# Kernel optimization log

Hardware: AMD Instinct MI355X
Metric: run time of the kernel (lower is better)

Reference implementation:

```python
import jax, jax.numpy as jnp
import numpy as np

# Static config (matches init_kwargs)
B = 1
D = 1024          # model_dim
H = 16            # num_heads
HD = 64           # head_dim
TPF = 256         # tokens_per_frame = latent_height*latent_width
LH, LW = 16, 16
FRAMES = 13
PREFIX = 1
ATTN = 3
CHUNKS = 4
TXT = 226                 # text_length per chunk
SEQ_TXT = CHUNKS * TXT    # 904
VID_LEN = FRAMES * TPF    # 3328
CHUNK_VID = (PREFIX + ATTN) * TPF  # 1024 video tokens per attention chunk
THETA = 10000.0
EPS = 1e-6
SCALE = 1.0 / np.sqrt(HD)
DT, DHE, DW = 16, 24, 24  # 3D rope split of head_dim


def setup_inputs() -> dict:
    key = jax.random.key(0)
    ks = jax.random.split(key, 16)
    def w(k, shape, s=0.02):
        return (jax.random.normal(k, shape) * s).astype(jnp.float32)
    return dict(
        vid_emb=jax.random.normal(ks[0], (B, VID_LEN, D), jnp.float32),
        text_emb=jax.random.normal(ks[1], (B, SEQ_TXT, D), jnp.float32),
        Wq=w(ks[2], (D, D)), bq=jnp.zeros((D,), jnp.float32),
        Wk=w(ks[3], (D, D)), bk=jnp.zeros((D,), jnp.float32),
        Wv=w(ks[4], (D, D)), bv=jnp.zeros((D,), jnp.float32),
        Wo=w(ks[5], (D, D)), bo=jnp.zeros((D,), jnp.float32),
        qn_w=jnp.ones((HD,), jnp.float32), qn_b=jnp.zeros((HD,), jnp.float32),
        kn_w=jnp.ones((HD,), jnp.float32), kn_b=jnp.zeros((HD,), jnp.float32),
        ssm_Win=w(ks[6], (D, D)), ssm_Wout=w(ks[7], (D, D)),
        ssm_gate=jnp.zeros((D,), jnp.float32),
        fg_t=jnp.full((D,), 0.1, jnp.float32), fg_v=jnp.full((D,), 0.1, jnp.float32),
        bg_t=jnp.full((D,), 0.1, jnp.float32), bg_v=jnp.full((D,), 0.1, jnp.float32),
    )


def _layernorm(x, w, b):
    mu = jnp.mean(x, axis=-1, keepdims=True)
    var = jnp.mean((x - mu) ** 2, axis=-1, keepdims=True)
    return (x - mu) * jax.lax.rsqrt(var + EPS) * w + b


def _rope_angles():
    # per-video-token 3D positions within a chunk
    tok = jnp.arange(CHUNK_VID)
    f = (tok // TPF).astype(jnp.float32)
    rem = tok % TPF
    hp = (rem // LW).astype(jnp.float32)
    wp = (rem % LW).astype(jnp.float32)
    def inv(d):
        return THETA ** (-jnp.arange(0, d, 2, dtype=jnp.float32) / d)
    return f[:, None] * inv(DT), hp[:, None] * inv(DHE), wp[:, None] * inv(DW)


def _rot(x, ang):
    half = x.shape[-1] // 2
    c, s = jnp.cos(ang), jnp.sin(ang)
    x1, x2 = x[..., :half], x[..., half:]
    return jnp.concatenate([x1 * c - x2 * s, x1 * s + x2 * c], axis=-1)


def _apply_rope3d(x, angs):
    at, ah, aw = angs
    return jnp.concatenate([
        _rot(x[..., :DT], at),
        _rot(x[..., DT:DT + DHE], ah),
        _rot(x[..., DT + DHE:], aw),
    ], axis=-1)


def _attn_forward(vid_emb, text_emb, Wq, bq, Wk, bk, Wv, bv, Wo, bo, qn_w, qn_b, kn_w, kn_b):
    b = vid_emb.shape[0]
    starts = np.arange(CHUNKS) * ATTN * TPF
    idx = jnp.asarray(starts)[:, None] + jnp.arange(CHUNK_VID)[None, :]  # [C, CHUNK_VID]
    txt_chunks = text_emb.reshape(b, CHUNKS, TXT, D)
    vid_chunks = vid_emb[:, idx]                                          # [b, C, CHUNK_VID, D]
    cur = jnp.concatenate([txt_chunks, vid_chunks], axis=2)               # [b, C, T, D]
    T = TXT + CHUNK_VID
    cur = cur.reshape(b * CHUNKS, T, D)

    def heads(x):
        return x.reshape(b * CHUNKS, T, H, HD).transpose(0, 2, 1, 3)      # [bc, h, t, d]

    q = _layernorm(heads(cur @ Wq + bq), qn_w, qn_b)
    k = _layernorm(heads(cur @ Wk + bk), kn_w, kn_b)
    v = heads(cur @ Wv + bv)

    angs = _rope_angles()
    q = jnp.concatenate([q[:, :, :TXT], _apply_rope3d(q[:, :, TXT:], angs)], axis=2)
    k = jnp.concatenate([k[:, :, :TXT], _apply_rope3d(k[:, :, TXT:], angs)], axis=2)

    scores = jnp.einsum('bhqd,bhkd->bhqk', q, k) * SCALE
    attn = jax.nn.softmax(scores, axis=-1)
    out = jnp.einsum('bhqk,bhkd->bhqd', attn, v)
    out = out.transpose(0, 2, 1, 3).reshape(b * CHUNKS, T, D) @ Wo + bo
    out = out.reshape(b, CHUNKS, T, D)

    text_out = out[:, :, :TXT].reshape(b, SEQ_TXT, D)
    vid_part = out[:, :, TXT:]                                            # [b, C, CHUNK_VID, D]
    vid_acc = jnp.zeros((b, VID_LEN, D), vid_emb.dtype).at[:, idx].add(vid_part)
    cnt = jnp.zeros((b, VID_LEN, 1), vid_emb.dtype).at[:, idx].add(jnp.ones((b, CHUNKS, CHUNK_VID, 1), vid_emb.dtype))
    vid_out = vid_acc / cnt
    return jnp.concatenate([text_out, vid_out], axis=1)


def _ssm(x, Win, Wout, gate_logit):
    # simplified TTT stand-in: gated linear recurrence h_t = g*h_{t-1} + u_t (causal scan)
    g = jax.nn.sigmoid(gate_logit)
    u = x @ Win
    a = jnp.broadcast_to(g, u.shape)
    def comb(c1, c2):
        a1, b1 = c1
        a2, b2 = c2
        return a1 * a2, a2 * b1 + b2
    _, h = jax.lax.associative_scan(comb, (a, u), axis=1)
    return h @ Wout


def _rev_text_chunks(t):
    b = t.shape[0]
    return jnp.flip(t.reshape(b, CHUNKS, TXT, D), axis=1).reshape(b, SEQ_TXT, D)


def _ssm_forward(emb, ssm_Win, ssm_Wout, ssm_gate, fg_t, fg_v, bg_t, bg_v):
    Ttxt = SEQ_TXT
    res = emb
    y = _ssm(emb, ssm_Win, ssm_Wout, ssm_gate)
    emb = res + jnp.concatenate([jnp.tanh(fg_t) * y[:, :Ttxt], jnp.tanh(fg_v) * y[:, Ttxt:]], axis=1)
    res2 = emb
    # multiscene reverse: flip text chunk order and video token order
    rev = jnp.concatenate([_rev_text_chunks(emb[:, :Ttxt]), jnp.flip(emb[:, Ttxt:], axis=1)], axis=1)
    y2 = _ssm(rev, ssm_Win, ssm_Wout, ssm_gate)
    y2 = jnp.concatenate([_rev_text_chunks(y2[:, :Ttxt]), jnp.flip(y2[:, Ttxt:], axis=1)], axis=1)
    return res2 + jnp.concatenate([jnp.tanh(bg_t) * y2[:, :Ttxt], jnp.tanh(bg_v) * y2[:, Ttxt:]], axis=1)


def reference(vid_emb, text_emb, Wq, bq, Wk, bk, Wv, bv, Wo, bo, qn_w, qn_b, kn_w, kn_b,
              ssm_Win, ssm_Wout, ssm_gate, fg_t, fg_v, bg_t, bg_v):
    emb = _attn_forward(vid_emb, text_emb, Wq, bq, Wk, bk, Wv, bv, Wo, bo, qn_w, qn_b, kn_w, kn_b)
    out = _ssm_forward(emb, ssm_Win, ssm_Wout, ssm_gate, fg_t, fg_v, bg_t, bg_v)
    return out[:, SEQ_TXT:], out[:, :SEQ_TXT]
```

## Files before the change

### kernel.cpp

```cpp
#include <hip/hip_runtime.h>
#include <cstdint>

constexpr int Dm       = 1024;
constexpr int Hh       = 16;
constexpr int HD       = 64;
constexpr int CHUNKS   = 4;
constexpr int TXT      = 226;
constexpr int SEQ_TXT  = 904;
constexpr int VID_LEN  = 3328;
constexpr int CHUNK_VID= 1024;
constexpr int Tt       = 1250;
constexpr int Tp       = 1280;
constexpr int M_QKV    = 5000;
constexpr int SEQm     = 4232;
constexpr int STRIDE_V = 768;
constexpr float EPSc   = 1e-6f;
constexpr float SCALEc = 0.125f;
constexpr float OFFS   = 8.0f;
constexpr float C16    = 1.6609640474f;
constexpr float C24    = 1.1073093649f;

constexpr int SEGL2 = 64;
constexpr int HALO  = 64;
constexpr int NSEG2 = (SEQm + SEGL2 - 1) / SEGL2;

typedef __attribute__((ext_vector_type(8))) short bf16x8;
typedef __attribute__((ext_vector_type(4))) float f32x4;

__device__ __forceinline__ ushort f2bf(float x) {
    uint32_t u = __float_as_uint(x);
    u += 0x7FFFu + ((u >> 16) & 1u);
    return (ushort)(u >> 16);
}
__device__ __forceinline__ float bf2f(ushort b) {
    return __uint_as_float(((uint32_t)b) << 16);
}

__device__ __forceinline__ void gload_lds16(const ushort* g, ushort* l) {
    __builtin_amdgcn_global_load_lds(
        (const __attribute__((address_space(1))) unsigned int*)g,
        (__attribute__((address_space(3))) unsigned int*)l, 16, 0, 0);
}

__device__ __forceinline__ int rev_map(int i) {
    if (i < SEQ_TXT) {
        int c = i / TXT, o = i - c * TXT;
        return (CHUNKS - 1 - c) * TXT + o;
    }
    int j = i - SEQ_TXT;
    return SEQ_TXT + (VID_LEN - 1 - j);
}

__global__ __launch_bounds__(256) void prep_all(
    const float* __restrict__ Wq, const float* __restrict__ Wk,
    const float* __restrict__ Wv, const float* __restrict__ Wo,
    const float* __restrict__ Win, const float* __restrict__ Wout,
    const float* __restrict__ vid, const float* __restrict__ txt,
    ushort* __restrict__ WqkvH, ushort* __restrict__ WqkvL,
    ushort* __restrict__ WoH, ushort* __restrict__ WoL,
    ushort* __restrict__ WinH, ushort* __restrict__ WinL,
    ushort* __restrict__ WoutH, ushort* __restrict__ WoutL,
    ushort* __restrict__ chi, ushort* __restrict__ clo) {
    __shared__ float tile[32][33];
    if (blockIdx.z == 6) {
        int base = (blockIdx.y * 32 + blockIdx.x) * 256 + threadIdx.x;
        for (int idx = base; idx < M_QKV * 256; idx += 32 * 32 * 256) {
            int row = idx >> 8, c4 = (idx & 255) * 4;
            int c = row / Tt, t = row - c * Tt;
            float4 x;
            if (t < TXT)
                x = *(const float4*)(txt + (size_t)(c * TXT + t) * Dm + c4);
            else
                x = *(const float4*)(vid + (size_t)(c * STRIDE_V + (t - TXT)) * Dm + c4);
            float v[4] = {x.x, x.y, x.z, x.w};
            ushort4 h, l;
            h.x = f2bf(v[0]); l.x = f2bf(v[0] - bf2f(h.x));
            h.y = f2bf(v[1]); l.y = f2bf(v[1] - bf2f(h.y));
            h.z = f2bf(v[2]); l.z = f2bf(v[2] - bf2f(h.z));
            h.w = f2bf(v[3]); l.w = f2bf(v[3] - bf2f(h.w));
            *(ushort4*)(chi + (size_t)row * Dm + c4) = h;
            *(ushort4*)(clo + (size_t)row * Dm + c4) = l;
        }
        return;
    }
    const float* W; ushort* Thi; ushort* Tlo;
    switch (blockIdx.z) {
        case 0: W = Wq;  Thi = WqkvH;               Tlo = WqkvL;               break;
        case 1: W = Wk;  Thi = WqkvH + 1024*1024;   Tlo = WqkvL + 1024*1024;   break;
        case 2: W = Wv;  Thi = WqkvH + 2*1024*1024; Tlo = WqkvL + 2*1024*1024; break;
        case 3: W = Wo;  Thi = WoH;   Tlo = WoL;   break;
        case 4: W = Win; Thi = WinH;  Tlo = WinL;  break;
        default:W = Wout;Thi = WoutH; Tlo = WoutL; break;
    }
    int k0 = blockIdx.y * 32, n0 = blockIdx.x * 32;
    int j = threadIdx.x & 31, i0 = threadIdx.x >> 5;
#pragma unroll
    for (int i = i0; i < 32; i += 8)
        tile[i][j] = W[(size_t)(k0 + i) * 1024 + n0 + j];
    __syncthreads();
#pragma unroll
    for (int i = i0; i < 32; i += 8) {
        float v = tile[j][i];
        ushort h = f2bf(v);
        size_t o = (size_t)(n0 + i) * 1024 + k0 + j;
        Thi[o] = h;
        Tlo[o] = f2bf(v - bf2f(h));
    }
}

template<int MODE>
__global__ __launch_bounds__(256) void gemm_sk(
    const ushort* __restrict__ Ahi, const ushort* __restrict__ Alo,
    const ushort* __restrict__ Bhi, const ushort* __restrict__ Blo,
    const float* __restrict__ f1, const float* __restrict__ f2,
    const float* __restrict__ f3,
    float* __restrict__ Cf, ushort* __restrict__ u1,
    int M, int N) {
    __shared__ ushort AHL[128 * 64];
    __shared__ ushort BHL[128 * 64];
    const int tid = threadIdx.x;
    const int w = tid >> 6, lane = tid & 63;
    const int lrow = lane & 15, quad = lane >> 4;
    const int mBase = blockIdx.y * 128, nBase = blockIdx.x * 128;

    const bool isB = (w >= 2);
    const int half = w & 1;
    const ushort* Phi = isB ? Bhi : Ahi;
    const ushort* Plo = isB ? Blo : Alo;
    ushort* lds = (isB ? BHL : AHL) + half * 4096;
    const int baseR = (isB ? nBase : mBase) + half * 64;
    const int maxr = (isB ? N : M) - 1;
    const int rl8 = lane >> 3;
    const int c = (lane & 7) ^ rl8;
    const ushort* Psel = (c < 4) ? Phi : Plo;
    const ushort* gb[8];
#pragma unroll
    for (int u = 0; u < 8; ++u) {
        int rg = min(baseR + u * 8 + rl8, maxr);
        gb[u] = Psel + (size_t)rg * 1024 + (c & 3) * 8;
    }

    const int mo = (w >> 1) * 64, no = (w & 1) * 64;
    const int p = quad ^ (lrow & 7);
    f32x4 acc[4][4];
#pragma unroll
    for (int i = 0; i < 4; ++i)
#pragma unroll
        for (int j = 0; j < 4; ++j) acc[i][j] = (f32x4){0.f, 0.f, 0.f, 0.f};

    const int kk0 = (MODE == 5) ? blockIdx.z * 512 : 0;
    const int kk1 = (MODE == 5) ? kk0 + 512 : 1024;
    for (int kk = kk0; kk < kk1; kk += 32) {
        __syncthreads();
#pragma unroll
        for (int u = 0; u < 8; ++u) gload_lds16(gb[u] + kk, lds + u * 512);
        __syncthreads();

        bf16x8 ah[4], al[4], bh[4], bl[4];
#pragma unroll
        for (int i = 0; i < 4; ++i) {
            int m = mo + i * 16 + lrow;
            ah[i] = *(const bf16x8*)&AHL[m * 64 + p * 8];
            al[i] = *(const bf16x8*)&AHL[m * 64 + (p ^ 4) * 8];
        }
#pragma unroll
        for (int j = 0; j < 4; ++j) {
            int n = no + j * 16 + lrow;
            bh[j] = *(const bf16x8*)&BHL[n * 64 + p * 8];
            bl[j] = *(const bf16x8*)&BHL[n * 64 + (p ^ 4) * 8];
        }
#pragma unroll
        for (int i = 0; i < 4; ++i)
#pragma unroll
            for (int j = 0; j < 4; ++j) {
                f32x4 a = acc[i][j];
                a = __builtin_amdgcn_mfma_f32_16x16x32_bf16(ah[i], bh[j], a, 0, 0, 0);
                a = __builtin_amdgcn_mfma_f32_16x16x32_bf16(al[i], bh[j], a, 0, 0, 0);
                a = __builtin_amdgcn_mfma_f32_16x16x32_bf16(ah[i], bl[j], a, 0, 0, 0);
                acc[i][j] = a;
            }
    }

    const size_t zoff = (MODE == 5) ? (size_t)blockIdx.z * M * N : 0;
#pragma unroll
    for (int i = 0; i < 4; ++i)
#pragma unroll
        for (int j = 0; j < 4; ++j) {
            const int col = nBase + no + j * 16 + lrow;
            float bv = 0.f;
            if constexpr (MODE == 1)
                bv = (col < 1024) ? f1[col]
                   : (col < 2048) ? f2[col - 1024] : f3[col - 2048];
#pragma unroll
            for (int r = 0; r < 4; ++r) {
                const int row = mBase + mo + i * 16 + quad * 4 + r;
                if (row >= M) continue;
                const size_t idx = (size_t)row * N + col;
                const float a = acc[i][j][r];
                if constexpr (MODE == 1) {
                    u1[idx] = f2bf(a + bv);
                } else {
                    Cf[zoff + idx] = a;
                }
            }
        }
}

__global__ __launch_bounds__(256) void lnrope(
    const ushort* __restrict__ qkvb,
    const float* __restrict__ qn_w, const float* __restrict__ qn_b,
    const float* __restrict__ kn_w, const float* __restrict__ kn_b,
    ushort* __restrict__ qP, ushort* __restrict__ kP, ushort* __restrict__ vT) {
    __shared__ ushort vtile[64][72];
    const int ch = blockIdx.y, c = ch >> 4, h = ch & 15;
    const int t0 = blockIdx.x * 64;
    const int tid = threadIdx.x, w = tid >> 6, lane = tid & 63;

    auto wsum = [](float x) {
#pragma unroll
        for (int o = 32; o; o >>= 1) x += __shfl_xor(x, o);
        return x;
    };

#pragma unroll 1
    for (int it = 0; it < 16; ++it) {
        const int tl = w * 16 + it;
        const int t = t0 + tl;
        ushort qb = 0, kb = 0, vb = 0;
        if (t < Tt) {
            size_t src = (size_t)(c * Tt + t) * 3072 + h * HD + lane;
            float qv = bf2f(qkvb[src]);
            float kv = bf2f(qkvb[src + 1024]);
            float vv = bf2f(qkvb[src + 2048]);

            float qmu = wsum(qv) * (1.f / 64.f);
            float qd  = qv - qmu;
            float qvar = wsum(qd * qd) * (1.f / 64.f);
            float qn = qd * rsqrtf(qvar + EPSc) * qn_w[lane] + qn_b[lane];

            float kmu = wsum(kv) * (1.f / 64.f);
            float kd  = kv - kmu;
            float kvar = wsum(kd * kd) * (1.f / 64.f);
            float kn = kd * rsqrtf(kvar + EPSc) * kn_w[lane] + kn_b[lane];

            if (t >= TXT) {
                int pos = t - TXT;
                int f = pos >> 8, rem2 = pos & 255, hp = rem2 >> 4, wp = rem2 & 15;
                int p, dl; float cc;
                if (lane < 16)      { cc = C16; p = f;  dl = lane; }
                else if (lane < 40) { cc = C24; p = hp; dl = lane - 16; }
                else                { cc = C24; p = wp; dl = lane - 40; }
                int halfd = (lane < 16) ? 8 : 12;
                int i = (dl < halfd) ? dl : dl - halfd;
                float ang = (float)p * exp2f(-(float)i * cc);
                float cs = cosf(ang), sn = sinf(ang);
                int partner = (dl < halfd) ? (lane + halfd) : (lane - halfd);
                float qo = __shfl(qn, partner);
                float ko = __shfl(kn, partner);
                qn = (dl < halfd) ? (qn * cs - qo * sn) : (qo * sn + qn * cs);
                kn = (dl < halfd) ? (kn * cs - ko * sn) : (ko * sn + kn * cs);
            }
            qb = f2bf(qn * SCALEc);
            kb = f2bf(kn);
            vb = f2bf(vv);
        }
        size_t dst = ((size_t)ch * Tp + t) * HD + lane;
        qP[dst] = qb;
        kP[dst] = kb;
        vtile[tl][lane] = vb;
    }
    __syncthreads();
    const int r = tid >> 2, ck = tid & 3;
    ushort* dst = vT + ((size_t)ch * HD + r) * Tp + t0;
    short o1[8], o2[8];
#pragma unroll
    for (int j = 0; j < 8; ++j) {
        o1[j] = (short)vtile[ck * 8 + j][r];
        o2[j] = (short)vtile[(ck + 4) * 8 + j][r];
    }
    *(bf16x8*)(dst + ck * 8)       = *(bf16x8*)o1;
    *(bf16x8*)(dst + (ck + 4) * 8) = *(bf16x8*)o2;
}

__global__ __launch_bounds__(256) void attn_mfma(
    const ushort* __restrict__ qP, const ushort* __restrict__ kP,
    const ushort* __restrict__ vT,
    ushort* __restrict__ ohi, ushort* __restrict__ olo) {
    const int ch = blockIdx.y;
    const int c = ch >> 4, h = ch & 15;
    const int qbase = blockIdx.x * 64;
    const int tid = threadIdx.x, w = tid >> 6, lane = tid & 63;
    const int lrow = lane & 15, quad = lane >> 4;

    __shared__ ushort KT[2][32 * 64];
    __shared__ ushort VTs[2][64 * 32];
    __shared__ ushort PB[4][16][40];

    const ushort* kg = kP + (size_t)ch * Tp * HD;
    const ushort* vg = vT + (size_t)ch * HD * Tp;

    const ushort* kgl = kg + (size_t)(w * 8 + (lane >> 3)) * HD
                           + ((lane & 7) ^ ((lane >> 3) & 7)) * 8;
    const ushort* vgl = vg + (size_t)(w * 16 + (lane >> 2)) * Tp + (lane & 3) * 8;

    const int qr = qbase + w * 16 + lrow;
    const ushort* qgp = qP + ((size_t)ch * Tp + qr) * HD + quad * 8;
    bf16x8 qf0 = *(const bf16x8*)qgp;
    bf16x8 qf1 = *(const bf16x8*)(qgp + 32);

    f32x4 accO[4];
#pragma unroll
    for (int dt = 0; dt < 4; ++dt) accO[dt] = (f32x4){0.f, 0.f, 0.f, 0.f};
    float lacc[4] = {0.f, 0.f, 0.f, 0.f};

    gload_lds16(kgl, &KT[0][w * 512]);
    gload_lds16(vgl, &VTs[0][w * 512]);

    const int NSTEP = Tp / 32;
    for (int s = 0; s < NSTEP; ++s) {
        const int b = s & 1;
        __syncthreads();
        if (s + 1 < NSTEP) {
            int kb = (s + 1) * 32;
            gload_lds16(kgl + (size_t)kb * HD, &KT[1 - b][w * 512]);
            gload_lds16(vgl + kb, &VTs[1 - b][w * 512]);
        }

        const int sw = lrow & 7;
        const ushort* r0 = &KT[b][lrow * 64];
        const ushort* r1 = &KT[b][(16 + lrow) * 64];
        bf16x8 k00 = *(const bf16x8*)(r0 + (quad ^ sw) * 8);
        bf16x8 k01 = *(const bf16x8*)(r0 + ((4 + quad) ^ sw) * 8);
        bf16x8 k10 = *(const bf16x8*)(r1 + (quad ^ sw) * 8);
        bf16x8 k11 = *(const bf16x8*)(r1 + ((4 + quad) ^ sw) * 8);
        f32x4 s0 = (f32x4){0.f, 0.f, 0.f, 0.f}, s1 = s0;
        s0 = __builtin_amdgcn_mfma_f32_16x16x32_bf16(qf0, k00, s0, 0, 0, 0);
        s0 = __builtin_amdgcn_mfma_f32_16x16x32_bf16(qf1, k01, s0, 0, 0, 0);
        s1 = __builtin_amdgcn_mfma_f32_16x16x32_bf16(qf0, k10, s1, 0, 0, 0);
        s1 = __builtin_amdgcn_mfma_f32_16x16x32_bf16(qf1, k11, s1, 0, 0, 0);

#pragma unroll
        for (int r = 0; r < 4; ++r) {
            float p0 = __expf(s0[r] - OFFS);
            float p1 = __expf(s1[r] - OFFS);
            lacc[r] += p0 + p1;
            int row = quad * 4 + r;
            PB[w][row][lrow]      = f2bf(p0);
            PB[w][row][16 + lrow] = f2bf(p1);
        }

        bf16x8 pf = *(const bf16x8*)&PB[w][lrow][quad * 8];
#pragma unroll
        for (int dt = 0; dt < 4; ++dt) {
            bf16x8 vf = *(const bf16x8*)&VTs[b][(dt * 16 + lrow) * 32 + quad * 8];
            accO[dt] = __builtin_amdgcn_mfma_f32_16x16x32_bf16(pf, vf, accO[dt], 0, 0, 0);
        }
    }

    float il[4];
#pragma unroll
    for (int r = 0; r < 4; ++r) {
        float l = lacc[r];
        l += __shfl_xor(l, 1);
        l += __shfl_xor(l, 2);
        l += __shfl_xor(l, 4);
        l += __shfl_xor(l, 8);
        l -= (float)(Tp - Tt) * __expf(-OFFS);
        il[r] = 1.f / l;
    }
#pragma unroll
    for (int dt = 0; dt < 4; ++dt)
#pragma unroll
        for (int r = 0; r < 4; ++r) {
            int qrow = qbase + w * 16 + quad * 4 + r;
            if (qrow < Tt) {
                float val = accO[dt][r] * il[r];
                size_t o = (size_t)(c * Tt + qrow) * Dm + h * HD + dt * 16 + lrow;
                ushort hv = f2bf(val);
                ohi[o] = hv;
                olo[o] = f2bf(val - bf2f(hv));
            }
        }
}

__global__ __launch_bounds__(256) void reduce_scatter(
    const float* __restrict__ P0, const float* __restrict__ bo,
    ushort* __restrict__ ehi, ushort* __restrict__ elo) {
    const float* P1 = P0 + (size_t)M_QKV * Dm;
    int idx = blockIdx.x * 256 + threadIdx.x;
    int row = idx >> 8, c4 = (idx & 255) * 4;
    float sx, sy, sz, sw;
    if (row < SEQ_TXT) {
        int c = row / TXT, t = row - c * TXT;
        size_t o = (size_t)(c * Tt + t) * Dm + c4;
        float4 a = *(const float4*)(P0 + o);
        float4 b = *(const float4*)(P1 + o);
        sx = a.x + b.x; sy = a.y + b.y; sz = a.z + b.z; sw = a.w + b.w;
    } else {
        int p = row - SEQ_TXT;
        sx = sy = sz = sw = 0.f; int cnt = 0;
#pragma unroll
        for (int c = 0; c < CHUNKS; ++c) {
            int off = p - c * STRIDE_V;
            if (off >= 0 && off < CHUNK_VID) {
                size_t o = (size_t)(c * Tt + TXT + off) * Dm + c4;
                float4 a = *(const float4*)(P0 + o);
                float4 b = *(const float4*)(P1 + o);
                sx += a.x + b.x; sy += a.y + b.y;
                sz += a.z + b.z; sw += a.w + b.w;
                ++cnt;
            }
        }
        float inv = 1.f / (float)cnt;
        sx *= inv; sy *= inv; sz *= inv; sw *= inv;
    }
    float4 b4 = *(const float4*)(bo + c4);
    float v[4] = {sx + b4.x, sy + b4.y, sz + b4.z, sw + b4.w};
    ushort4 h, l;
    h.x = f2bf(v[0]); l.x = f2bf(v[0] - bf2f(h.x));
    h.y = f2bf(v[1]); l.y = f2bf(v[1] - bf2f(h.y));
    h.z = f2bf(v[2]); l.z = f2bf(v[2] - bf2f(h.z));
    h.w = f2bf(v[3]); l.w = f2bf(v[3] - bf2f(h.w));
    *(ushort4*)(ehi + (size_t)row * Dm + c4) = h;
    *(ushort4*)(elo + (size_t)row * Dm + c4) = l;
}

__global__ __launch_bounds__(256) void scan_halo(
    const float* __restrict__ P0, const float* __restrict__ gate,
    ushort* __restrict__ hhi, ushort* __restrict__ hlo, int perm) {
    const float* P1 = P0 + (size_t)SEQm * Dm;
    int ch = blockIdx.x * 256 + threadIdx.x;
    int seg = blockIdx.y;
    float g = 1.f / (1.f + expf(-gate[ch]));
    int tw0 = seg * SEGL2;
    int tw1 = min(SEQm, tw0 + SEGL2);
    int t0 = max(0, tw0 - HALO);
    float hv = 0.f;
    for (int t = t0; t < tw0; ++t) {
        int rt = perm ? rev_map(t) : t;
        size_t o = (size_t)rt * Dm + ch;
        hv = fmaf(g, hv, P0[o] + P1[o]);
    }
    for (int t = tw0; t < tw1; ++t) {
        int rt = perm ? rev_map(t) : t;
        size_t o = (size_t)rt * Dm + ch;
        hv = fmaf(g, hv, P0[o] + P1[o]);
        ushort h = f2bf(hv);
        hhi[o] = h;
        hlo[o] = f2bf(hv - bf2f(h));
    }
}

__global__ __launch_bounds__(256) void reduce_c1(
    const float* __restrict__ P0,
    const ushort* __restrict__ ehi, const ushort* __restrict__ elo,
    const float* __restrict__ fg_t, const float* __restrict__ fg_v,
    float* __restrict__ emb2, ushort* __restrict__ e2hi, ushort* __restrict__ e2lo) {
    const float* P1 = P0 + (size_t)SEQm * Dm;
    int idx = blockIdx.x * 256 + threadIdx.x;
    int row = idx >> 8, c4 = (idx & 255) * 4;
    const float* fg = (row < SEQ_TXT) ? fg_t : fg_v;
    size_t o = (size_t)row * Dm + c4;
    float4 a = *(const float4*)(P0 + o);
    float4 b = *(const float4*)(P1 + o);
    ushort4 eh = *(const ushort4*)(ehi + o);
    ushort4 el = *(const ushort4*)(elo + o);
    float v[4];
    v[0] = (bf2f(eh.x) + bf2f(el.x)) + tanhf(fg[c4 + 0]) * (a.x + b.x);
    v[1] = (bf2f(eh.y) + bf2f(el.y)) + tanhf(fg[c4 + 1]) * (a.y + b.y);
    v[2] = (bf2f(eh.z) + bf2f(el.z)) + tanhf(fg[c4 + 2]) * (a.z + b.z);
    v[3] = (bf2f(eh.w) + bf2f(el.w)) + tanhf(fg[c4 + 3]) * (a.w + b.w);
    *(float4*)(emb2 + o) = make_float4(v[0], v[1], v[2], v[3]);
    ushort4 h, l;
    h.x = f2bf(v[0]); l.x = f2bf(v[0] - bf2f(h.x));
    h.y = f2bf(v[1]); l.y = f2bf(v[1] - bf2f(h.y));
    h.z = f2bf(v[2]); l.z = f2bf(v[2] - bf2f(h.z));
    h.w = f2bf(v[3]); l.w = f2bf(v[3] - bf2f(h.w));
    *(ushort4*)(e2hi + o) = h;
    *(ushort4*)(e2lo + o) = l;
}

__global__ __launch_bounds__(256) void reduce_fin(
    const float* __restrict__ P0, const float* __restrict__ emb2,
    const float* __restrict__ bg_t, const float* __restrict__ bg_v,
    float* __restrict__ outp) {
    const float* P1 = P0 + (size_t)SEQm * Dm;
    int idx = blockIdx.x * 256 + threadIdx.x;
    int row = idx >> 8, c4 = (idx & 255) * 4;
    const float* bg = (row < SEQ_TXT) ? bg_t : bg_v;
    int drow = (row >= SEQ_TXT) ? (row - SEQ_TXT) : (VID_LEN + row);
    size_t o = (size_t)row * Dm + c4;
    float4 a = *(const float4*)(P0 + o);
    float4 b = *(const float4*)(P1 + o);
    float4 e = *(const float4*)(emb2 + o);
    float4 r = make_float4(e.x + tanhf(bg[c4 + 0]) * (a.x + b.x),
                           e.y + tanhf(bg[c4 + 1]) * (a.y + b.y),
                           e.z + tanhf(bg[c4 + 2]) * (a.z + b.z),
                           e.w + tanhf(bg[c4 + 3]) * (a.w + b.w));
    *(float4*)(outp + (size_t)drow * Dm + c4) = r;
}

extern "C" void kernel_launch(void* const* d_in, const int* in_sizes, int n_in,
                              void* d_out, int out_size, void* d_ws, size_t ws_size,
                              hipStream_t stream) {
    const float* vid_emb = (const float*)d_in[0];
    const float* text_emb= (const float*)d_in[1];
    const float* Wq = (const float*)d_in[2];  const float* bq = (const float*)d_in[3];
    const float* Wk = (const float*)d_in[4];  const float* bk = (const float*)d_in[5];
    const float* Wv = (const float*)d_in[6];  const float* bv = (const float*)d_in[7];
    const float* Wo = (const float*)d_in[8];  const float* bo = (const float*)d_in[9];
    const float* qn_w = (const float*)d_in[10]; const float* qn_b = (const float*)d_in[11];
    const float* kn_w = (const float*)d_in[12]; const float* kn_b = (const float*)d_in[13];
    const float* Win  = (const float*)d_in[14]; const float* Wout = (const float*)d_in[15];
    const float* gate = (const float*)d_in[16];
    const float* fg_t = (const float*)d_in[17]; const float* fg_v = (const float*)d_in[18];
    const float* bg_t = (const float*)d_in[19]; const float* bg_v = (const float*)d_in[20];

    char* W8 = (char*)d_ws;
    if (ws_size < 128647168u) return;
    ushort* WqkvH = (ushort*)(W8 + 0);
    ushort* WqkvL = (ushort*)(W8 + 6291456);
    ushort* WoH   = (ushort*)(W8 + 12582912);
    ushort* WoL   = (ushort*)(W8 + 14680064);
    ushort* WinH  = (ushort*)(W8 + 16777216);
    ushort* WinL  = (ushort*)(W8 + 18874368);
    ushort* WoutH = (ushort*)(W8 + 20971520);
    ushort* WoutL = (ushort*)(W8 + 23068672);
    ushort* qkvb  = (ushort*)(W8 + 25165824);
    ushort* curH  = (ushort*)(W8 + 55885824);
    ushort* curL  = (ushort*)(W8 + 66125824);
    ushort* qPl   = (ushort*)(W8 + 76365824);
    ushort* kPl   = (ushort*)(W8 + 86851584);
    ushort* vTl   = (ushort*)(W8 + 97337344);
    ushort* aoutH = (ushort*)(W8 + 25165824);
    ushort* aoutL = (ushort*)(W8 + 35405824);
    float*  PWo   = (float*) (W8 + 76365824);
    ushort* embH  = (ushort*)(W8 + 45645824);
    ushort* embL  = (ushort*)(W8 + 54312960);
    float*  PW    = (float*) (W8 + 76365824);
    ushort* hbufH = (ushort*)(W8 + 25165824);
    ushort* hbufL = (ushort*)(W8 + 33832960);
    float*  emb2  = (float*) (W8 + 111034368);
    ushort* e2H   = (ushort*)(W8 + 25165824);
    ushort* e2L   = (ushort*)(W8 + 33832960);
    ushort* hbuf2H= (ushort*)(W8 + 45645824);
    ushort* hbuf2L= (ushort*)(W8 + 54312960);
    float*  outp  = (float*)d_out;

    prep_all<<<dim3(32, 32, 7), 256, 0, stream>>>(
        Wq, Wk, Wv, Wo, Win, Wout, vid_emb, text_emb,
        WqkvH, WqkvL, WoH, WoL, WinH, WinL, WoutH, WoutL, curH, curL);

    gemm_sk<1><<<dim3(24, 40), 256, 0, stream>>>(
        curH, curL, WqkvH, WqkvL, bq, bk, bv, nullptr, qkvb, M_QKV, 3072);

    lnrope<<<dim3(Tp / 64, 64), 256, 0, stream>>>(qkvb, qn_w, qn_b, kn_w, kn_b,
                                                  qPl, kPl, vTl);

    attn_mfma<<<dim3(Tp / 64, 64), 256, 0, stream>>>(qPl, kPl, vTl, aoutH, aoutL);

    gemm_sk<5><<<dim3(8, 40, 2), 256, 0, stream>>>(
        aoutH, aoutL, WoH, WoL, nullptr, nullptr, nullptr, PWo, nullptr,
        M_QKV, 1024);
    reduce_scatter<<<SEQm, 256, 0, stream>>>(PWo, bo, embH, embL);

    dim3 gsq(8, 34, 2);
    dim3 gscan(Dm / 256, NSEG2);

    gemm_sk<5><<<gsq, 256, 0, stream>>>(
        embH, embL, WinH, WinL, nullptr, nullptr, nullptr, PW, nullptr,
        SEQm, 1024);
    scan_halo<<<gscan, 256, 0, stream>>>(PW, gate, hbufH, hbufL, 0);
    gemm_sk<5><<<gsq, 256, 0, stream>>>(
        hbufH, hbufL, WoutH, WoutL, nullptr, nullptr, nullptr, PW, nullptr,
        SEQm, 1024);
    reduce_c1<<<SEQm, 256, 0, stream>>>(PW, embH, embL, fg_t, fg_v,
                                        emb2, e2H, e2L);

    gemm_sk<5><<<gsq, 256, 0, stream>>>(
        e2H, e2L, WinH, WinL, nullptr, nullptr, nullptr, PW, nullptr,
        SEQm, 1024);
    scan_halo<<<gscan, 256, 0, stream>>>(PW, gate, hbuf2H, hbuf2L, 1);
    gemm_sk<5><<<gsq, 256, 0, stream>>>(
        hbuf2H, hbuf2L, WoutH, WoutL, nullptr, nullptr, nullptr, PW, nullptr,
        SEQm, 1024);
    reduce_fin<<<SEQm, 256, 0, stream>>>(PW, emb2, bg_t, bg_v, outp);
}
```

Baseline: 672.2 us.

## Add 256x256-tile eight-phase pipelined QKV GEMM kernel with direct-to-LDS loads

Replaces the generic split-precision QKV GEMM with a dedicated kernel using 512 threads and 256x256 output tiles. It double-buffers LDS in half-tiles and interleaves global-to-LDS staging with MFMA phases under barriers and setprio. The K loop covers 48 steps that walk the hi/lo split-precision planes. The larger tiles cut global traffic per output, and the finer-grained schedule is meant to hide load latency. In exchange the grid shrinks to 240 blocks, which may underfill the GPU, and LDS use grows to 128KB per block.

```diff
diff --git a/kernel.cpp b/kernel.cpp
--- a/kernel.cpp
+++ b/kernel.cpp
@@ -204,6 +204,180 @@
                 }
             }
         }
+}
+
+__global__ __launch_bounds__(512, 2) void gemm_qkv_8ph(
+    const ushort* __restrict__ Ahi, const ushort* __restrict__ Alo,
+    const ushort* __restrict__ Bhi, const ushort* __restrict__ Blo,
+    const float* __restrict__ f1, const float* __restrict__ f2,
+    const float* __restrict__ f3, ushort* __restrict__ out) {
+    constexpr int Mq  = M_QKV;
+    constexpr int Nq  = 3072;
+    constexpr int NKT = 48;
+
+    __shared__ __align__(16) ushort ldsq[65536];
+
+    const int tid = threadIdx.x;
+    const int w = tid >> 6, lane = tid & 63;
+    const int lrow = lane & 15, quad = lane >> 4;
+    const int wr = w >> 2, wc = w & 3;
+    const int mBase = blockIdx.y * 256, nBase = blockIdx.x * 256;
+
+    uint32_t offA[2][2], offB[2][2];
+#pragma unroll
+    for (int q = 0; q < 2; ++q) {
+        const int s  = q * 512 + tid;
+        const int sr = s >> 3;
+        const int c  = (s & 7) ^ (sr & 7);
+        const int ra = (sr >> 6) * 128 + (sr & 63);
+        const int rb = (sr >> 5) * 64 + (sr & 31);
+#pragma unroll
+        for (int h = 0; h < 2; ++h) {
+            offA[q][h] = (uint32_t)(min(mBase + ra + h * 64, Mq - 1) * 1024 + c * 8);
+            offB[q][h] = (uint32_t)((nBase + rb + h * 32) * 1024 + c * 8);
+        }
+    }
+    const int ldsW = w * 512;
+
+    const int pA0 = quad ^ (lrow & 7);
+    const int pA1 = (4 + quad) ^ (lrow & 7);
+    const int arow = wr * 64 + lrow;
+    const int brow = wc * 32 + lrow;
+
+    f32x4 acc[8][4];
+#pragma unroll
+    for (int i = 0; i < 8; ++i)
+#pragma unroll
+        for (int j = 0; j < 4; ++j) acc[i][j] = (f32x4){0.f, 0.f, 0.f, 0.f};
+
+    bf16x8 af[8];
+    bf16x8 bfr[4];
+
+#define STAGE_A(b, h, kt) do { \
+        const ushort* pl_ = (((kt) >> 4) == 1 ? Alo : Ahi) + (((kt) & 15) * 64); \
+        ushort* d_ = &ldsq[((b) * 2 + (h)) * 8192 + ldsW]; \
+        gload_lds16(pl_ + offA[0][(h)], d_); \
+        gload_lds16(pl_ + offA[1][(h)], d_ + 4096); \
+    } while (0)
+#define STAGE_B(b, h, kt) do { \
+        const ushort* pl_ = (((kt) >> 4) == 2 ? Blo : Bhi) + (((kt) & 15) * 64); \
+        ushort* d_ = &ldsq[32768 + ((b) * 2 + (h)) * 8192 + ldsW]; \
+        gload_lds16(pl_ + offB[0][(h)], d_); \
+        gload_lds16(pl_ + offB[1][(h)], d_ + 4096); \
+    } while (0)
+#define LD_A(b, h) do { \
+        const ushort* ba_ = &ldsq[((b) * 2 + (h)) * 8192]; \
+        af[0] = *(const bf16x8*)(ba_ + (arow +  0) * 64 + pA0 * 8); \
+        af[1] = *(const bf16x8*)(ba_ + (arow +  0) * 64 + pA1 * 8); \
+        af[2] = *(const bf16x8*)(ba_ + (arow + 16) * 64 + pA0 * 8); \
+        af[3] = *(const bf16x8*)(ba_ + (arow + 16) * 64 + pA1 * 8); \
+        af[4] = *(const bf16x8*)(ba_ + (arow + 32) * 64 + pA0 * 8); \
+        af[5] = *(const bf16x8*)(ba_ + (arow + 32) * 64 + pA1 * 8); \
+        af[6] = *(const bf16x8*)(ba_ + (arow + 48) * 64 + pA0 * 8); \
+        af[7] = *(const bf16x8*)(ba_ + (arow + 48) * 64 + pA1 * 8); \
+    } while (0)
+#define LD_B(b, h) do { \
+        const ushort* bb_ = &ldsq[32768 + ((b) * 2 + (h)) * 8192]; \
+        bfr[0] = *(const bf16x8*)(bb_ + (brow +  0) * 64 + pA0 * 8); \
+        bfr[1] = *(const bf16x8*)(bb_ + (brow +  0) * 64 + pA1 * 8); \
+        bfr[2] = *(const bf16x8*)(bb_ + (brow + 16) * 64 + pA0 * 8); \
+        bfr[3] = *(const bf16x8*)(bb_ + (brow + 16) * 64 + pA1 * 8); \
+    } while (0)
+#define MMO(mh, nh, i, ks) \
+        acc[(mh)*4+(i)][(nh)*2+0] = __builtin_amdgcn_mfma_f32_16x16x32_bf16( \
+            af[(i)*2+(ks)], bfr[0+(ks)], acc[(mh)*4+(i)][(nh)*2+0], 0, 0, 0); \
+        acc[(mh)*4+(i)][(nh)*2+1] = __builtin_amdgcn_mfma_f32_16x16x32_bf16( \
+            af[(i)*2+(ks)], bfr[2+(ks)], acc[(mh)*4+(i)][(nh)*2+1], 0, 0, 0);
+#define MM16(mh, nh) do { \
+        __builtin_amdgcn_s_setprio(1); \
+        MMO(mh, nh, 0, 0) MMO(mh, nh, 1, 0) MMO(mh, nh, 2, 0) MMO(mh, nh, 3, 0) \
+        MMO(mh, nh, 0, 1) MMO(mh, nh, 1, 1) MMO(mh, nh, 2, 1) MMO(mh, nh, 3, 1) \
+        __builtin_amdgcn_s_setprio(0); \
+    } while (0)
+#define BAR()  __builtin_amdgcn_s_barrier()
+#define LGK0() asm volatile("s_waitcnt lgkmcnt(0)" ::: "memory")
+#define VMC4() asm volatile("s_waitcnt vmcnt(4)" ::: "memory")
+
+    STAGE_A(0, 0, 0); STAGE_B(0, 1, 0); STAGE_B(0, 0, 0); STAGE_A(0, 1, 0);
+    STAGE_A(1, 0, 1); STAGE_B(1, 1, 1);
+    VMC4();
+    BAR();
+
+#pragma unroll 1
+    for (int t = 0; t < NKT / 2; ++t) {
+        const int kt1  = 2 * t + 1;
+        const int ktn0 = min(2 * t + 2, NKT - 1);
+        const int ktn1 = min(2 * t + 3, NKT - 1);
+        LD_A(0, 0); LD_B(0, 0);
+        STAGE_B(1, 0, kt1);
+        BAR(); LGK0();
+        MM16(0, 0);
+        BAR();
+        LD_B(0, 1);
+        STAGE_A(1, 1, kt1);
+        BAR(); LGK0();
+        MM16(0, 1);
+        BAR();
+        LD_A(0, 1);
+        STAGE_A(0, 0, ktn0);
+        BAR(); LGK0();
+        MM16(1, 1);
+        BAR();
+        LD_B(0, 0);
+        STAGE_B(0, 1, ktn0);
+        BAR(); LGK0();
+        MM16(1, 0);
+        VMC4();
+        BAR();
+        LD_A(1, 0); LD_B(1, 0);
+        STAGE_B(0, 0, ktn0);
+        BAR(); LGK0();
+        MM16(0, 0);
+        BAR();
+        LD_B(1, 1);
+        STAGE_A(0, 1, ktn0);
+        BAR(); LGK0();
+        MM16(0, 1);
+        BAR();
+        LD_A(1, 1);
+        STAGE_A(1, 0, ktn1);
+        BAR(); LGK0();
+        MM16(1, 1);
+        BAR();
+        LD_B(1, 0);
+        STAGE_B(1, 1, ktn1);
+        BAR(); LGK0();
+        MM16(1, 0);
+        VMC4();
+        BAR();
+    }
+    asm volatile("s_waitcnt vmcnt(0)" ::: "memory");
+
+#undef STAGE_A
+#undef STAGE_B
+#undef LD_A
+#undef LD_B
+#undef MMO
+#undef MM16
+#undef BAR
+#undef LGK0
+#undef VMC4
+
+#pragma unroll
+    for (int i = 0; i < 8; ++i) {
+#pragma unroll
+        for (int j = 0; j < 4; ++j) {
+            const int col = nBase + wc * 64 + j * 16 + lrow;
+            const float bias = (col < 1024) ? f1[col]
+                             : (col < 2048) ? f2[col - 1024] : f3[col - 2048];
+#pragma unroll
+            for (int r = 0; r < 4; ++r) {
+                const int row = mBase + wr * 128 + i * 16 + quad * 4 + r;
+                if (row < Mq)
+                    out[(size_t)row * Nq + col] = f2bf(acc[i][j][r] + bias);
+            }
+        }
+    }
 }
 
 __global__ __launch_bounds__(256) void lnrope(
@@ -551,8 +725,8 @@
         Wq, Wk, Wv, Wo, Win, Wout, vid_emb, text_emb,
         WqkvH, WqkvL, WoH, WoL, WinH, WinL, WoutH, WoutL, curH, curL);
 
-    gemm_sk<1><<<dim3(24, 40), 256, 0, stream>>>(
-        curH, curL, WqkvH, WqkvL, bq, bk, bv, nullptr, qkvb, M_QKV, 3072);
+    gemm_qkv_8ph<<<dim3(12, 20), 512, 0, stream>>>(
+        curH, curL, WqkvH, WqkvL, bq, bk, bv, qkvb);
 
     lnrope<<<dim3(Tp / 64, 64), 256, 0, stream>>>(qkvb, qn_w, qn_b, kn_w, kn_b,
                                                   qPl, kPl, vTl);
```

Result: no change. 660.5 us (-1.7%).

## Replace QKV GEMM with 256x256-tile 512-thread double-buffered MFMA kernel

Applied to the files above, without the earlier changes.

Adds a dedicated QKV projection kernel that uses 256x256 output tiles per 512-thread block, in place of the generic split-bf16 GEMM with smaller tiles. Global data is staged straight into LDS through an XOR-swizzled, double-buffered pipeline, and the MFMA block runs at raised wave priority. The larger tiles are meant to improve operand reuse and reduce global traffic. In exchange the grid drops to 240 blocks with heavy register and 128KB LDS use, which may lower occupancy and leave part of the GPU underfilled.

```diff
diff --git a/kernel.cpp b/kernel.cpp
--- a/kernel.cpp
+++ b/kernel.cpp
@@ -204,6 +204,121 @@
                 }
             }
         }
+}
+
+__global__ __launch_bounds__(512, 2) void gemm_qkv_8ph(
+    const ushort* __restrict__ Ahi, const ushort* __restrict__ Alo,
+    const ushort* __restrict__ Bhi, const ushort* __restrict__ Blo,
+    const float* __restrict__ f1, const float* __restrict__ f2,
+    const float* __restrict__ f3, ushort* __restrict__ out) {
+    constexpr int Mq  = M_QKV;
+    constexpr int Nq  = 3072;
+    constexpr int NSL = 32;
+
+    __shared__ __align__(16) ushort ldsq[65536];
+
+    const int tid = threadIdx.x;
+    const int w = tid >> 6, lane = tid & 63;
+    const int lrow = lane & 15, quad = lane >> 4;
+    const int wr = w >> 2, wc = w & 3;
+    const int mBase = blockIdx.y * 256, nBase = blockIdx.x * 256;
+
+    const int cA = (tid & 7) ^ ((tid >> 3) & 7);
+    const ushort* pA = (cA < 4) ? Ahi : Alo;
+    const ushort* pB = (cA < 4) ? Bhi : Blo;
+    uint32_t offA[4], offB[4];
+#pragma unroll
+    for (int q = 0; q < 4; ++q) {
+        const int r = q * 64 + (tid >> 3);
+        offA[q] = (uint32_t)(min(mBase + r, Mq - 1) * 1024 + (cA & 3) * 8);
+        offB[q] = (uint32_t)((nBase + r) * 1024 + (cA & 3) * 8);
+    }
+    const int ldsW = w * 512;
+
+    const int pH = quad ^ (lrow & 7);
+    const int arow = wr * 128 + lrow;
+    const int brow = wc * 64 + lrow;
+
+    f32x4 acc[8][4];
+#pragma unroll
+    for (int i = 0; i < 8; ++i)
+#pragma unroll
+        for (int j = 0; j < 4; ++j) acc[i][j] = (f32x4){0.f, 0.f, 0.f, 0.f};
+
+#define STAGE_AB(b, s) do { \
+        ushort* dA_ = ldsq + (b) * 16384 + ldsW; \
+        ushort* dB_ = ldsq + 32768 + (b) * 16384 + ldsW; \
+        const uint32_t ko_ = (uint32_t)(s) * 32u; \
+        gload_lds16(pA + offA[0] + ko_, dA_); \
+        gload_lds16(pA + offA[1] + ko_, dA_ + 4096); \
+        gload_lds16(pA + offA[2] + ko_, dA_ + 8192); \
+        gload_lds16(pA + offA[3] + ko_, dA_ + 12288); \
+        gload_lds16(pB + offB[0] + ko_, dB_); \
+        gload_lds16(pB + offB[1] + ko_, dB_ + 4096); \
+        gload_lds16(pB + offB[2] + ko_, dB_ + 8192); \
+        gload_lds16(pB + offB[3] + ko_, dB_ + 12288); \
+    } while (0)
+
+    STAGE_AB(0, 0);
+    asm volatile("s_waitcnt vmcnt(0)" ::: "memory");
+    __builtin_amdgcn_s_barrier();
+
+#pragma unroll 1
+    for (int s = 0; s < NSL; ++s) {
+        const int b = s & 1;
+        if (s + 1 < NSL) STAGE_AB(1 - b, s + 1);
+
+        const ushort* aB_ = ldsq + b * 16384;
+        const ushort* bB_ = ldsq + 32768 + b * 16384;
+        bf16x8 ahi[8], alo[8], bhi[4], blo[4];
+#pragma unroll
+        for (int i = 0; i < 8; ++i) {
+            const ushort* rp = aB_ + (arow + i * 16) * 64;
+            ahi[i] = *(const bf16x8*)(rp + pH * 8);
+            alo[i] = *(const bf16x8*)(rp + (pH ^ 4) * 8);
+        }
+#pragma unroll
+        for (int j = 0; j < 4; ++j) {
+            const ushort* rp = bB_ + (brow + j * 16) * 64;
+            bhi[j] = *(const bf16x8*)(rp + pH * 8);
+            blo[j] = *(const bf16x8*)(rp + (pH ^ 4) * 8);
+        }
+
+        __builtin_amdgcn_s_barrier();
+        asm volatile("s_waitcnt lgkmcnt(0)" ::: "memory");
+        __builtin_amdgcn_s_setprio(1);
+#pragma unroll
+        for (int i = 0; i < 8; ++i)
+#pragma unroll
+            for (int j = 0; j < 4; ++j) {
+                f32x4 a = acc[i][j];
+                a = __builtin_amdgcn_mfma_f32_16x16x32_bf16(ahi[i], bhi[j], a, 0, 0, 0);
+                a = __builtin_amdgcn_mfma_f32_16x16x32_bf16(alo[i], bhi[j], a, 0, 0, 0);
+                a = __builtin_amdgcn_mfma_f32_16x16x32_bf16(ahi[i], blo[j], a, 0, 0, 0);
+                acc[i][j] = a;
+            }
+        __builtin_amdgcn_s_setprio(0);
+        asm volatile("s_waitcnt vmcnt(0)" ::: "memory");
+        __builtin_amdgcn_s_barrier();
+    }
+
+#undef STAGE_AB
+
+#pragma unroll
+    for (int i = 0; i < 8; ++i) {
+#pragma unroll
+        for (int j = 0; j < 4; ++j) {
+            const int col = nBase + wc * 64 + j * 16 + lrow;
+            const float bias = (col < 1024) ? f1[col]
+                             : (col < 2048) ? f2[col - 1024] : f3[col - 2048];
+#pragma unroll
+            for (int r = 0; r < 4; ++r) {
+                const int row = mBase + wr * 128 + i * 16 + quad * 4 + r;
+                if (row < Mq)
+                    out[(size_t)row * Nq + col] = f2bf(acc[i][j][r] + bias);
+            }
+        }
+    }
 }
 
 __global__ __launch_bounds__(256) void lnrope(
@@ -551,8 +666,8 @@
         Wq, Wk, Wv, Wo, Win, Wout, vid_emb, text_emb,
         WqkvH, WqkvL, WoH, WoL, WinH, WinL, WoutH, WoutL, curH, curL);
 
-    gemm_sk<1><<<dim3(24, 40), 256, 0, stream>>>(
-        curH, curL, WqkvH, WqkvL, bq, bk, bv, nullptr, qkvb, M_QKV, 3072);
+    gemm_qkv_8ph<<<dim3(12, 20), 512, 0, stream>>>(
+        curH, curL, WqkvH, WqkvL, bq, bk, bv, qkvb);
 
     lnrope<<<dim3(Tp / 64, 64), 256, 0, stream>>>(qkvb, qn_w, qn_b, kn_w, kn_b,
                                                   qPl, kPl, vTl);
```

New measurement: 656.5 us. 1.02x faster.
